# Kernel optimization log

Hardware: AMD Instinct MI355X
Metric: run time of the kernel (lower is better)

## Reference

```python
import jax, jax.numpy as jnp
import numpy as np

N_NODES = 100000
N_EDGES = 1_600_000
IN_CH = 64
HID = 128
OUT_CH = 2


def _glorot(key, shape):
    fan_in = shape[0]
    return jax.random.normal(key, shape, dtype=jnp.float32) / jnp.sqrt(jnp.float32(fan_in))


def setup_inputs() -> dict:
    key = jax.random.key(0)
    ks = jax.random.split(key, 10)
    x = jax.random.normal(ks[0], (N_NODES, IN_CH), dtype=jnp.float32)
    edge_index = jax.random.randint(ks[1], (2, N_EDGES), 0, N_NODES, dtype=jnp.int64)
    # SAGEConv layer 0: lin_l (neighbor, with bias) + lin_r (root)
    W_n0 = _glorot(ks[2], (IN_CH, HID))
    W_s0 = _glorot(ks[3], (IN_CH, HID))
    b0 = jnp.zeros((HID,), dtype=jnp.float32)
    # SAGEConv layer 1
    W_n1 = _glorot(ks[4], (HID, HID))
    W_s1 = _glorot(ks[5], (HID, HID))
    b1 = jnp.zeros((HID,), dtype=jnp.float32)
    # final fc
    fc_w = _glorot(ks[6], (HID, OUT_CH))
    fc_b = jnp.zeros((OUT_CH,), dtype=jnp.float32)
    return {"x": x, "edge_index": edge_index, "W_n0": W_n0, "W_s0": W_s0, "b0": b0,
            "W_n1": W_n1, "W_s1": W_s1, "b1": b1, "fc_w": fc_w, "fc_b": fc_b}


def _sage_conv(h, src, dst, W_n, W_s, b, num_nodes):
    # mean aggregation of source features onto destination nodes
    agg = jax.ops.segment_sum(h[src], dst, num_segments=num_nodes)  # [N, d]
    cnt = jax.ops.segment_sum(jnp.ones_like(dst, dtype=h.dtype), dst, num_segments=num_nodes)
    mean = agg / jnp.maximum(cnt, 1.0)[:, None]
    return mean @ W_n + h @ W_s + b


def reference(x, edge_index, W_n0, W_s0, b0, W_n1, W_s1, b1, fc_w, fc_b):
    src, dst = edge_index[0], edge_index[1]
    n = x.shape[0]
    h = jax.nn.relu(_sage_conv(x, src, dst, W_n0, W_s0, b0, n))  # dropout is identity in eval mode
    h = jax.nn.relu(_sage_conv(h, src, dst, W_n1, W_s1, b1, n))
    return h @ fc_w + fc_b
```

## Files before the change

### kernel.cpp

```cpp
#include <hip/hip_runtime.h>

#define N_NODES 100000
#define IN_CH 64
#define HID 128
#define BSH 8
#define NBUCK ((N_NODES + 255) >> 8)
#define NCB 512

typedef short short8 __attribute__((ext_vector_type(8)));
typedef float floatx4 __attribute__((ext_vector_type(4)));
typedef float floatx2 __attribute__((ext_vector_type(2)));

__device__ __forceinline__ unsigned short f2bf(float f) {
    unsigned u = __builtin_bit_cast(unsigned, f);
    u += 0x7fffu + ((u >> 16) & 1u);
    return (unsigned short)(u >> 16);
}

template <int K>
__device__ __forceinline__ void pack_dev(const float* __restrict__ Wn,
                                         const float* __restrict__ Ws,
                                         unsigned short* __restrict__ Bpack, int idx) {
    int s = idx >> 9;
    int rem = idx & 511;
    int t = rem >> 6;
    int lane = rem & 63;
    int quad = lane >> 4;
    int n = t * 16 + (lane & 15);
    unsigned short v[8];
#pragma unroll
    for (int j = 0; j < 8; ++j) {
        int k = s * 32 + quad * 8 + j;
        float w = (k < K) ? Wn[(size_t)k * HID + n] : Ws[(size_t)(k - K) * HID + n];
        v[j] = f2bf(w);
    }
    *(short8*)(Bpack + (size_t)idx * 8) = *(short8*)v;
}

__global__ __launch_bounds__(256) void histprep_kernel(const int* __restrict__ dst,
                                                       int* __restrict__ table, int E, int chunk,
                                                       const float* __restrict__ x,
                                                       unsigned short* __restrict__ x_bf,
                                                       unsigned char* __restrict__ x_f8,
                                                       const float* __restrict__ Wn0,
                                                       const float* __restrict__ Ws0,
                                                       unsigned short* __restrict__ Bpack0,
                                                       const float* __restrict__ Wn1,
                                                       const float* __restrict__ Ws1,
                                                       unsigned short* __restrict__ Bpack1,
                                                       int* __restrict__ scan_done, int n4) {
    int b = blockIdx.x;
    if (b < NCB) {
        if (b == 0 && threadIdx.x == 0) *scan_done = 0;
        __shared__ int h[NBUCK];
        for (int i = threadIdx.x; i < NBUCK; i += 256) h[i] = 0;
        __syncthreads();
        int e0 = b * chunk;
        int e1 = min(E, e0 + chunk);
        for (int e = e0 + threadIdx.x; e < e1; e += 256) atomicAdd(&h[dst[e] >> BSH], 1);
        __syncthreads();
        for (int i = threadIdx.x; i < NBUCK; i += 256) table[i * NCB + b] = h[i];
    } else if (b < NCB + 8) {
        pack_dev<IN_CH>(Wn0, Ws0, Bpack0, (b - NCB) * 256 + threadIdx.x);
    } else if (b < NCB + 24) {
        pack_dev<HID>(Wn1, Ws1, Bpack1, (b - NCB - 8) * 256 + threadIdx.x);
    } else {
        int i = (b - NCB - 24) * 256 + threadIdx.x;
        if (i < n4) {
            float4 v = ((const float4*)x)[i];
            ushort4 o;
            o.x = f2bf(v.x); o.y = f2bf(v.y); o.z = f2bf(v.z); o.w = f2bf(v.w);
            ((ushort4*)x_bf)[i] = o;
            int p8 = __builtin_amdgcn_cvt_pk_fp8_f32(v.x, v.y, 0, false);
            p8 = __builtin_amdgcn_cvt_pk_fp8_f32(v.z, v.w, p8, true);
            ((unsigned*)x_f8)[i] = (unsigned)p8;
        }
    }
}

__global__ __launch_bounds__(256) void scan12_kernel(int* __restrict__ table,
                                                     int* __restrict__ tot,
                                                     int* __restrict__ bstart,
                                                     int* __restrict__ ptr,
                                                     int* __restrict__ scan_done, int E) {
    __shared__ int s[256];
    __shared__ int lastflag;
    int b = blockIdx.x, t = threadIdx.x;
    int c0 = table[b * NCB + 2 * t];
    int c1 = table[b * NCB + 2 * t + 1];
    int s2 = c0 + c1;
    s[t] = s2;
    __syncthreads();
#pragma unroll
    for (int off = 1; off < 256; off <<= 1) {
        int v = (t >= off) ? s[t - off] : 0;
        __syncthreads();
        s[t] += v;
        __syncthreads();
    }
    int excl2 = s[t] - s2;
    table[b * NCB + 2 * t] = excl2;
    table[b * NCB + 2 * t + 1] = excl2 + c0;
    if (t == 255) {
        __hip_atomic_store(&tot[b], s[255], __ATOMIC_RELAXED, __HIP_MEMORY_SCOPE_AGENT);
        int prev = __hip_atomic_fetch_add(scan_done, 1, __ATOMIC_ACQ_REL, __HIP_MEMORY_SCOPE_AGENT);
        lastflag = (prev == NBUCK - 1);
    }
    __syncthreads();
    if (!lastflag) return;
    int v0 = (2 * t < NBUCK)
                 ? __hip_atomic_load(&tot[2 * t], __ATOMIC_RELAXED, __HIP_MEMORY_SCOPE_AGENT) : 0;
    int v1 = (2 * t + 1 < NBUCK)
                 ? __hip_atomic_load(&tot[2 * t + 1], __ATOMIC_RELAXED, __HIP_MEMORY_SCOPE_AGENT) : 0;
    int p2 = v0 + v1;
    __syncthreads();
    s[t] = p2;
    __syncthreads();
#pragma unroll
    for (int off = 1; off < 256; off <<= 1) {
        int u = (t >= off) ? s[t - off] : 0;
        __syncthreads();
        s[t] += u;
        __syncthreads();
    }
    int e2 = s[t] - p2;
    if (2 * t < NBUCK) bstart[2 * t] = e2;
    if (2 * t + 1 < NBUCK) bstart[2 * t + 1] = e2 + v0;
    if (t == 0) {
        bstart[NBUCK] = E;
        ptr[N_NODES] = E;
    }
}

__global__ __launch_bounds__(256) void bin_kernel(const int* __restrict__ src,
                                                  const int* __restrict__ dst,
                                                  const int* __restrict__ table,
                                                  const int* __restrict__ bstart,
                                                  unsigned* __restrict__ binned, int E, int chunk) {
    __shared__ int cur[NBUCK];
    int blk = blockIdx.x;
    for (int i = threadIdx.x; i < NBUCK; i += 256) cur[i] = bstart[i] + table[i * NCB + blk];
    __syncthreads();
    int e0 = blk * chunk;
    int e1 = min(E, e0 + chunk);
    for (int e = e0 + threadIdx.x; e < e1; e += 256) {
        int d = dst[e];
        int b = d >> BSH;
        int pos = atomicAdd(&cur[b], 1);
        if ((unsigned)pos < (unsigned)E)
            binned[pos] = (unsigned)src[e] | ((unsigned)(d & 255) << 17);
    }
}

__global__ __launch_bounds__(256) void place_kernel(const unsigned* __restrict__ binned,
                                                    const int* __restrict__ bstart,
                                                    int* __restrict__ ptr,
                                                    int* __restrict__ sorted, int N, int E) {
    __shared__ int deg[256];
    __shared__ int cur[256];
    __shared__ int ssum[256];
    int b = blockIdx.x, t = threadIdx.x;
    int start = bstart[b], end = bstart[b + 1];
    start = max(0, min(start, E));
    end = max(start, min(end, E));
    deg[t] = 0;
    __syncthreads();
    for (int i = start + t; i < end; i += 256) atomicAdd(&deg[(binned[i] >> 17) & 255], 1);
    __syncthreads();
    int a = deg[t];
    ssum[t] = a;
    __syncthreads();
#pragma unroll
    for (int off = 1; off < 256; off <<= 1) {
        int u = (t >= off) ? ssum[t - off] : 0;
        __syncthreads();
        ssum[t] += u;
        __syncthreads();
    }
    int excl = ssum[t] - a;
    cur[t] = excl;
    int n0 = b * 256 + t;
    if (n0 < N) ptr[n0] = start + excl;
    __syncthreads();
    for (int i = start + t; i < end; i += 256) {
        unsigned p = binned[i];
        int dl = (p >> 17) & 255;
        int pos = start + atomicAdd(&cur[dl], 1);
        if ((unsigned)pos < (unsigned)E) sorted[pos] = (int)(p & 0x1FFFF);
    }
}

template <int C>
__global__ __launch_bounds__(256) void gather_mean_w16p(const int* __restrict__ ptr,
                                                        const int* __restrict__ srcs,
                                                        const unsigned char* __restrict__ feat,
                                                        unsigned short* __restrict__ mean, int N,
                                                        int E) {
    constexpr int R = C / 16;
    constexpr int LOGR = (C == 64) ? 2 : 3;
    constexpr int NPW = 64 / R;
    const int lane = threadIdx.x & 63;
    const int g = lane >> LOGR;
    const int l = lane & (R - 1);
    const int w = (blockIdx.x * 4 + (threadIdx.x >> 6)) * NPW + g;
    if (w >= N) return;
    int s0 = ptr[w], s1 = ptr[w + 1];
    s0 = max(0, min(s0, E));
    s1 = max(s0, min(s1, E));
    const int deg = min(s1 - s0, 4096);

    floatx2 accq[4][8];
#pragma unroll
    for (int q = 0; q < 4; ++q)
#pragma unroll
        for (int u = 0; u < 8; ++u) { accq[q][u][0] = 0.0f; accq[q][u][1] = 0.0f; }

    const int nfull = deg & ~3;
    int j = 0;
    if (nfull > 0) {
        int cidn[4];
        uint4 v[4];
        {
            int cid0[4];
#pragma unroll
            for (int q = 0; q < 4; ++q)
                cid0[q] = (int)min((unsigned)srcs[s0 + q], (unsigned)(N_NODES - 1));
#pragma unroll
            for (int q = 0; q < 4; ++q)
                v[q] = *(const uint4*)(feat + (size_t)cid0[q] * C + l * 16);
            int base1 = (4 < nfull) ? s0 + 4 : s0;
#pragma unroll
            for (int q = 0; q < 4; ++q)
                cidn[q] = (int)min((unsigned)srcs[base1 + q], (unsigned)(N_NODES - 1));
        }
        for (; j < nfull; j += 4) {
            uint4 vn[4];
#pragma unroll
            for (int q = 0; q < 4; ++q)
                vn[q] = *(const uint4*)(feat + (size_t)cidn[q] * C + l * 16);
            int base2 = (j + 8 < nfull) ? s0 + j + 8 : s0;
            int cid2[4];
#pragma unroll
            for (int q = 0; q < 4; ++q)
                cid2[q] = (int)min((unsigned)srcs[base2 + q], (unsigned)(N_NODES - 1));
#pragma unroll
            for (int q = 0; q < 4; ++q) {
                const uint dw[4] = {v[q].x, v[q].y, v[q].z, v[q].w};
#pragma unroll
                for (int d = 0; d < 4; ++d) {
                    accq[q][2 * d + 0] += __builtin_amdgcn_cvt_pk_f32_fp8(dw[d], false);
                    accq[q][2 * d + 1] += __builtin_amdgcn_cvt_pk_f32_fp8(dw[d], true);
                }
            }
#pragma unroll
            for (int q = 0; q < 4; ++q) { v[q] = vn[q]; cidn[q] = cid2[q]; }
        }
    }
    if (j < deg) {
        int cid[4];
#pragma unroll
        for (int q = 0; q < 4; ++q) {
            int jj = min(j + q, deg - 1);
            cid[q] = (int)min((unsigned)srcs[s0 + jj], (unsigned)(N_NODES - 1));
        }
        uint4 v[4];
#pragma unroll
        for (int q = 0; q < 4; ++q)
            v[q] = *(const uint4*)(feat + (size_t)cid[q] * C + l * 16);
#pragma unroll
        for (int q = 0; q < 4; ++q) {
            uint dw[4] = {v[q].x, v[q].y, v[q].z, v[q].w};
#pragma unroll
            for (int d = 0; d < 4; ++d) dw[d] = (j + q < deg) ? dw[d] : 0u;
#pragma unroll
            for (int d = 0; d < 4; ++d) {
                accq[q][2 * d + 0] += __builtin_amdgcn_cvt_pk_f32_fp8(dw[d], false);
                accq[q][2 * d + 1] += __builtin_amdgcn_cvt_pk_f32_fp8(dw[d], true);
            }
        }
    }
#pragma unroll
    for (int u = 0; u < 8; ++u) {
        accq[0][u] += accq[1][u];
        accq[2][u] += accq[3][u];
        accq[0][u] += accq[2][u];
    }
    const float inv = (deg > 0) ? 1.0f / (float)deg : 0.0f;
    unsigned short o[16];
#pragma unroll
    for (int u = 0; u < 8; ++u) {
        o[2 * u + 0] = f2bf(accq[0][u][0] * inv);
        o[2 * u + 1] = f2bf(accq[0][u][1] * inv);
    }
    unsigned short* mp = mean + (size_t)w * C + l * 16;
    *(uint4*)(mp + 0) = ((const uint4*)o)[0];
    *(uint4*)(mp + 8) = ((const uint4*)o)[1];
}

template <int KT, bool FUSE_FC>
__global__ __launch_bounds__(256) void sage_gemm_mfma(const unsigned short* __restrict__ meanb,
                                                      const unsigned short* __restrict__ hb,
                                                      const unsigned short* __restrict__ Bpack,
                                                      const float* __restrict__ bias,
                                                      const float* __restrict__ fcw,
                                                      const float* __restrict__ fcb,
                                                      unsigned short* __restrict__ outb,
                                                      unsigned char* __restrict__ out8,
                                                      float* __restrict__ outf, int N) {
    constexpr int KH = KT / 2;
    constexpr int LDA = KT + 8;
    __shared__ unsigned short As[64 * LDA];
    const int t = threadIdx.x;
    const int row0 = blockIdx.x * 64;

    constexpr int SEGS = KT / 8;
    for (int c = t; c < 64 * SEGS; c += 256) {
        int r = c / SEGS, seg = c % SEGS;
        int rsrc = row0 + r;
        if (rsrc >= N) rsrc = N - 1;
        const unsigned short* srcp = (seg < SEGS / 2)
                                         ? meanb + (size_t)rsrc * KH + seg * 8
                                         : hb + (size_t)rsrc * KH + (seg - SEGS / 2) * 8;
        *(uint4*)&As[r * LDA + seg * 8] = *(const uint4*)srcp;
    }
    __syncthreads();

    const int lane = t & 63;
    const int wave = t >> 6;
    const int quad = lane >> 4;
    const int lo = lane & 15;

    floatx4 acc[8];
#pragma unroll
    for (int i = 0; i < 8; ++i)
#pragma unroll
        for (int r = 0; r < 4; ++r) acc[i][r] = 0.0f;

    const unsigned short* abase = &As[(wave * 16 + lo) * LDA + quad * 8];
#pragma unroll
    for (int s = 0; s < KT / 32; ++s) {
        short8 a = *(const short8*)(abase + s * 32);
        const short8* bp = (const short8*)Bpack + (size_t)(s * 8) * 64 + lane;
#pragma unroll
        for (int tt = 0; tt < 8; ++tt) {
            short8 b = bp[tt * 64];
            acc[tt] = __builtin_amdgcn_mfma_f32_16x16x32_bf16(a, b, acc[tt], 0, 0, 0);
        }
    }

    if (!FUSE_FC) {
        __syncthreads();
#pragma unroll
        for (int tt = 0; tt < 8; ++tt) {
            int col = tt * 16 + lo;
            float bv = bias[col];
#pragma unroll
            for (int r = 0; r < 4; ++r) {
                int rl = wave * 16 + quad * 4 + r;
                As[rl * LDA + col] = f2bf(fmaxf(acc[tt][r] + bv, 0.0f));
            }
        }
        __syncthreads();
        for (int i = t; i < 64 * (HID / 8); i += 256) {
            int r = i >> 4, ch = i & 15;
            int row = row0 + r;
            if (row < N)
                *(uint4*)(outb + (size_t)row * HID + ch * 8) = *(const uint4*)&As[r * LDA + ch * 8];
        }
        __syncthreads();
        unsigned char* As8 = (unsigned char*)As;
#pragma unroll
        for (int tt = 0; tt < 8; ++tt) {
            int col = tt * 16 + lo;
            float bv = bias[col];
#pragma unroll
            for (int r = 0; r < 4; ++r) {
                int rl = wave * 16 + quad * 4 + r;
                float v = fmaxf(acc[tt][r] + bv, 0.0f);
                int p8 = __builtin_amdgcn_cvt_pk_fp8_f32(v, v, 0, false);
                As8[rl * (LDA * 2) + col] = (unsigned char)(p8 & 0xff);
            }
        }
        __syncthreads();
        for (int i = t; i < 64 * (HID / 16); i += 256) {
            int r = i >> 3, ch = i & 7;
            int row = row0 + r;
            if (row < N)
                *(uint4*)(out8 + (size_t)row * HID + ch * 16) =
                    *(const uint4*)&As8[r * (LDA * 2) + ch * 16];
        }
    } else {
        float o0[4] = {}, o1[4] = {};
#pragma unroll
        for (int tt = 0; tt < 8; ++tt) {
            int col = tt * 16 + lo;
            float bv = bias[col];
            float w0 = fcw[col * 2 + 0];
            float w1 = fcw[col * 2 + 1];
#pragma unroll
            for (int r = 0; r < 4; ++r) {
                float v = fmaxf(acc[tt][r] + bv, 0.0f);
                o0[r] += v * w0;
                o1[r] += v * w1;
            }
        }
#pragma unroll
        for (int r = 0; r < 4; ++r) {
#pragma unroll
            for (int m = 8; m >= 1; m >>= 1) {
                o0[r] += __shfl_xor(o0[r], m, 16);
                o1[r] += __shfl_xor(o1[r], m, 16);
            }
        }
        if (lo == 0) {
#pragma unroll
            for (int r = 0; r < 4; ++r) {
                int row = row0 + wave * 16 + quad * 4 + r;
                if (row < N) {
                    outf[(size_t)row * 2 + 0] = o0[r] + fcb[0];
                    outf[(size_t)row * 2 + 1] = o1[r] + fcb[1];
                }
            }
        }
    }
}

extern "C" void kernel_launch(void* const* d_in, const int* in_sizes, int n_in,
                              void* d_out, int out_size, void* d_ws, size_t ws_size,
                              hipStream_t stream) {
    const float* x   = (const float*)d_in[0];
    const int*   ei  = (const int*)d_in[1];
    const float* Wn0 = (const float*)d_in[2];
    const float* Ws0 = (const float*)d_in[3];
    const float* b0  = (const float*)d_in[4];
    const float* Wn1 = (const float*)d_in[5];
    const float* Ws1 = (const float*)d_in[6];
    const float* b1  = (const float*)d_in[7];
    const float* fcw = (const float*)d_in[8];
    const float* fcb = (const float*)d_in[9];
    float* out = (float*)d_out;

    const int E = in_sizes[1] / 2;
    const int* src = ei;
    const int* dst = ei + E;
    const int N = N_NODES;
    const int chunk = (E + NCB - 1) / NCB;

    char* ws = (char*)d_ws;
    size_t off = 0;
    int* table  = (int*)(ws + off); off += (size_t)NBUCK * NCB * 4;
    int* tot    = (int*)(ws + off); off += 4096;
    int* bstart = (int*)(ws + off); off += 4096;
    int* scan_done = (int*)(ws + off); off += 256;
    int* ptr    = (int*)(ws + off); off += (size_t)(N + 1) * 4 + 60; off &= ~(size_t)63;
    unsigned* binned = (unsigned*)(ws + off); off += (size_t)E * 4;
    int* sorted = (int*)(ws + off); off += (size_t)E * 4;
    off = (off + 255) & ~(size_t)255;
    unsigned short* x_bf   = (unsigned short*)(ws + off); off += (size_t)N * IN_CH * 2;
    unsigned short* mean0  = (unsigned short*)(ws + off); off += (size_t)N * IN_CH * 2;
    unsigned short* h1_bf  = (unsigned short*)(ws + off); off += (size_t)N * HID * 2;
    unsigned short* mean1  = (unsigned short*)(ws + off); off += (size_t)N * HID * 2;
    unsigned char*  h1_f8  = (unsigned char*)(ws + off);  off += (size_t)N * HID;
    unsigned char*  x_f8   = (unsigned char*)(ws + off);  off += (size_t)N * IN_CH;
    off = (off + 255) & ~(size_t)255;
    unsigned short* Bpack0 = (unsigned short*)(ws + off); off += (size_t)(2 * IN_CH / 32) * 8 * 64 * 8 * 2;
    unsigned short* Bpack1 = (unsigned short*)(ws + off); off += (size_t)(2 * HID / 32) * 8 * 64 * 8 * 2;

    {
        int n4 = N * IN_CH / 4;
        int nblk = NCB + 24 + (n4 + 255) / 256;
        histprep_kernel<<<nblk, 256, 0, stream>>>(dst, table, E, chunk, x, x_bf, x_f8,
                                                  Wn0, Ws0, Bpack0, Wn1, Ws1, Bpack1,
                                                  scan_done, n4);
    }
    scan12_kernel<<<NBUCK, 256, 0, stream>>>(table, tot, bstart, ptr, scan_done, E);
    bin_kernel<<<NCB, 256, 0, stream>>>(src, dst, table, bstart, binned, E, chunk);
    place_kernel<<<NBUCK, 256, 0, stream>>>(binned, bstart, ptr, sorted, N, E);

    gather_mean_w16p<IN_CH><<<(N + 63) / 64, 256, 0, stream>>>(ptr, sorted, x_f8, mean0, N, E);
    sage_gemm_mfma<2 * IN_CH, false><<<(N + 63) / 64, 256, 0, stream>>>(
        mean0, x_bf, Bpack0, b0, nullptr, nullptr, h1_bf, h1_f8, nullptr, N);

    gather_mean_w16p<HID><<<(N + 31) / 32, 256, 0, stream>>>(ptr, sorted, h1_f8, mean1, N, E);
    sage_gemm_mfma<2 * HID, true><<<(N + 63) / 64, 256, 0, stream>>>(
        mean1, h1_bf, Bpack1, b1, fcw, fcb, nullptr, nullptr, out, N);
}
```

Measured before the change: 232.3 us.

## Replace two-level bucket sort CSR build with global-atomic count, alloc, scatter

```diff
diff --git a/kernel.cpp b/kernel.cpp
--- a/kernel.cpp
+++ b/kernel.cpp
@@ -3,9 +3,9 @@
 #define N_NODES 100000
 #define IN_CH 64
 #define HID 128
-#define BSH 8
-#define NBUCK ((N_NODES + 255) >> 8)
-#define NCB 512
+#define NCC 512
+#define ZB ((N_NODES + 1023) >> 10)
+#define NAB ((N_NODES + 255) >> 8)
 
 typedef short short8 __attribute__((ext_vector_type(8)));
 typedef float floatx4 __attribute__((ext_vector_type(4)));
@@ -37,35 +37,28 @@
     *(short8*)(Bpack + (size_t)idx * 8) = *(short8*)v;
 }
 
-__global__ __launch_bounds__(256) void histprep_kernel(const int* __restrict__ dst,
-                                                       int* __restrict__ table, int E, int chunk,
-                                                       const float* __restrict__ x,
-                                                       unsigned short* __restrict__ x_bf,
-                                                       unsigned char* __restrict__ x_f8,
-                                                       const float* __restrict__ Wn0,
-                                                       const float* __restrict__ Ws0,
-                                                       unsigned short* __restrict__ Bpack0,
-                                                       const float* __restrict__ Wn1,
-                                                       const float* __restrict__ Ws1,
-                                                       unsigned short* __restrict__ Bpack1,
-                                                       int* __restrict__ scan_done, int n4) {
+__global__ __launch_bounds__(256) void prep_kernel(const float* __restrict__ x,
+                                                   unsigned short* __restrict__ x_bf,
+                                                   unsigned char* __restrict__ x_f8,
+                                                   const float* __restrict__ Wn0,
+                                                   const float* __restrict__ Ws0,
+                                                   unsigned short* __restrict__ Bpack0,
+                                                   const float* __restrict__ Wn1,
+                                                   const float* __restrict__ Ws1,
+                                                   unsigned short* __restrict__ Bpack1,
+                                                   int* __restrict__ degcnt,
+                                                   int* __restrict__ gcur, int n4) {
     int b = blockIdx.x;
-    if (b < NCB) {
-        if (b == 0 && threadIdx.x == 0) *scan_done = 0;
-        __shared__ int h[NBUCK];
-        for (int i = threadIdx.x; i < NBUCK; i += 256) h[i] = 0;
-        __syncthreads();
-        int e0 = b * chunk;
-        int e1 = min(E, e0 + chunk);
-        for (int e = e0 + threadIdx.x; e < e1; e += 256) atomicAdd(&h[dst[e] >> BSH], 1);
-        __syncthreads();
-        for (int i = threadIdx.x; i < NBUCK; i += 256) table[i * NCB + b] = h[i];
-    } else if (b < NCB + 8) {
-        pack_dev<IN_CH>(Wn0, Ws0, Bpack0, (b - NCB) * 256 + threadIdx.x);
-    } else if (b < NCB + 24) {
-        pack_dev<HID>(Wn1, Ws1, Bpack1, (b - NCB - 8) * 256 + threadIdx.x);
+    if (b < ZB) {
+        if (b == 0 && threadIdx.x == 0) *gcur = 0;
+        int i = (b * 256 + threadIdx.x) * 4;
+        *(int4*)(degcnt + i) = make_int4(0, 0, 0, 0);
+    } else if (b < ZB + 8) {
+        pack_dev<IN_CH>(Wn0, Ws0, Bpack0, (b - ZB) * 256 + threadIdx.x);
+    } else if (b < ZB + 24) {
+        pack_dev<HID>(Wn1, Ws1, Bpack1, (b - ZB - 8) * 256 + threadIdx.x);
     } else {
-        int i = (b - NCB - 24) * 256 + threadIdx.x;
+        int i = (b - ZB - 24) * 256 + threadIdx.x;
         if (i < n4) {
             float4 v = ((const float4*)x)[i];
             ushort4 o;
@@ -78,120 +71,57 @@
     }
 }
 
-__global__ __launch_bounds__(256) void scan12_kernel(int* __restrict__ table,
-                                                     int* __restrict__ tot,
-                                                     int* __restrict__ bstart,
-                                                     int* __restrict__ ptr,
-                                                     int* __restrict__ scan_done, int E) {
-    __shared__ int s[256];
-    __shared__ int lastflag;
-    int b = blockIdx.x, t = threadIdx.x;
-    int c0 = table[b * NCB + 2 * t];
-    int c1 = table[b * NCB + 2 * t + 1];
-    int s2 = c0 + c1;
-    s[t] = s2;
+__global__ __launch_bounds__(256) void count_kernel(const int* __restrict__ dst,
+                                                    int* __restrict__ degcnt, int E, int chunk) {
+    int e0 = blockIdx.x * chunk;
+    int e1 = min(E, e0 + chunk);
+    for (int e = e0 + threadIdx.x; e < e1; e += 256) atomicAdd(&degcnt[dst[e]], 1);
+}
+
+__global__ __launch_bounds__(256) void alloc_kernel(const int* __restrict__ degcnt,
+                                                    int* __restrict__ gcur,
+                                                    int* __restrict__ ptr,
+                                                    int* __restrict__ cur, int N) {
+    __shared__ int ssum[256];
+    __shared__ int sbase;
+    int t = threadIdx.x;
+    int n = blockIdx.x * 256 + t;
+    int d = (n < N) ? degcnt[n] : 0;
+    d = max(0, min(d, 65535));
+    ssum[t] = d;
     __syncthreads();
 #pragma unroll
     for (int off = 1; off < 256; off <<= 1) {
-        int v = (t >= off) ? s[t - off] : 0;
-        __syncthreads();
-        s[t] += v;
-        __syncthreads();
-    }
-    int excl2 = s[t] - s2;
-    table[b * NCB + 2 * t] = excl2;
-    table[b * NCB + 2 * t + 1] = excl2 + c0;
-    if (t == 255) {
-        __hip_atomic_store(&tot[b], s[255], __ATOMIC_RELAXED, __HIP_MEMORY_SCOPE_AGENT);
-        int prev = __hip_atomic_fetch_add(scan_done, 1, __ATOMIC_ACQ_REL, __HIP_MEMORY_SCOPE_AGENT);
-        lastflag = (prev == NBUCK - 1);
-    }
+        int u = (t >= off) ? ssum[t - off] : 0;
+        __syncthreads();
+        ssum[t] += u;
+        __syncthreads();
+    }
+    int excl = ssum[t] - d;
+    if (t == 255) sbase = atomicAdd(gcur, ssum[255]);
     __syncthreads();
-    if (!lastflag) return;
-    int v0 = (2 * t < NBUCK)
-                 ? __hip_atomic_load(&tot[2 * t], __ATOMIC_RELAXED, __HIP_MEMORY_SCOPE_AGENT) : 0;
-    int v1 = (2 * t + 1 < NBUCK)
-                 ? __hip_atomic_load(&tot[2 * t + 1], __ATOMIC_RELAXED, __HIP_MEMORY_SCOPE_AGENT) : 0;
-    int p2 = v0 + v1;
-    __syncthreads();
-    s[t] = p2;
-    __syncthreads();
-#pragma unroll
-    for (int off = 1; off < 256; off <<= 1) {
-        int u = (t >= off) ? s[t - off] : 0;
-        __syncthreads();
-        s[t] += u;
-        __syncthreads();
-    }
-    int e2 = s[t] - p2;
-    if (2 * t < NBUCK) bstart[2 * t] = e2;
-    if (2 * t + 1 < NBUCK) bstart[2 * t + 1] = e2 + v0;
-    if (t == 0) {
-        bstart[NBUCK] = E;
-        ptr[N_NODES] = E;
-    }
-}
-
-__global__ __launch_bounds__(256) void bin_kernel(const int* __restrict__ src,
-                                                  const int* __restrict__ dst,
-                                                  const int* __restrict__ table,
-                                                  const int* __restrict__ bstart,
-                                                  unsigned* __restrict__ binned, int E, int chunk) {
-    __shared__ int cur[NBUCK];
-    int blk = blockIdx.x;
-    for (int i = threadIdx.x; i < NBUCK; i += 256) cur[i] = bstart[i] + table[i * NCB + blk];
-    __syncthreads();
-    int e0 = blk * chunk;
+    int p = sbase + excl;
+    if (n < N) {
+        ptr[n] = p;
+        cur[n] = p;
+    }
+}
+
+__global__ __launch_bounds__(256) void scatter_kernel(const int* __restrict__ src,
+                                                      const int* __restrict__ dst,
+                                                      int* __restrict__ cur,
+                                                      int* __restrict__ sorted, int E, int chunk) {
+    int e0 = blockIdx.x * chunk;
     int e1 = min(E, e0 + chunk);
     for (int e = e0 + threadIdx.x; e < e1; e += 256) {
-        int d = dst[e];
-        int b = d >> BSH;
-        int pos = atomicAdd(&cur[b], 1);
-        if ((unsigned)pos < (unsigned)E)
-            binned[pos] = (unsigned)src[e] | ((unsigned)(d & 255) << 17);
-    }
-}
-
-__global__ __launch_bounds__(256) void place_kernel(const unsigned* __restrict__ binned,
-                                                    const int* __restrict__ bstart,
-                                                    int* __restrict__ ptr,
-                                                    int* __restrict__ sorted, int N, int E) {
-    __shared__ int deg[256];
-    __shared__ int cur[256];
-    __shared__ int ssum[256];
-    int b = blockIdx.x, t = threadIdx.x;
-    int start = bstart[b], end = bstart[b + 1];
-    start = max(0, min(start, E));
-    end = max(start, min(end, E));
-    deg[t] = 0;
-    __syncthreads();
-    for (int i = start + t; i < end; i += 256) atomicAdd(&deg[(binned[i] >> 17) & 255], 1);
-    __syncthreads();
-    int a = deg[t];
-    ssum[t] = a;
-    __syncthreads();
-#pragma unroll
-    for (int off = 1; off < 256; off <<= 1) {
-        int u = (t >= off) ? ssum[t - off] : 0;
-        __syncthreads();
-        ssum[t] += u;
-        __syncthreads();
-    }
-    int excl = ssum[t] - a;
-    cur[t] = excl;
-    int n0 = b * 256 + t;
-    if (n0 < N) ptr[n0] = start + excl;
-    __syncthreads();
-    for (int i = start + t; i < end; i += 256) {
-        unsigned p = binned[i];
-        int dl = (p >> 17) & 255;
-        int pos = start + atomicAdd(&cur[dl], 1);
-        if ((unsigned)pos < (unsigned)E) sorted[pos] = (int)(p & 0x1FFFF);
+        int pos = atomicAdd(&cur[dst[e]], 1);
+        if ((unsigned)pos < (unsigned)E) sorted[pos] = src[e];
     }
 }
 
 template <int C>
 __global__ __launch_bounds__(256) void gather_mean_w16p(const int* __restrict__ ptr,
+                                                        const int* __restrict__ degcnt,
                                                         const int* __restrict__ srcs,
                                                         const unsigned char* __restrict__ feat,
                                                         unsigned short* __restrict__ mean, int N,
@@ -204,10 +134,10 @@
     const int l = lane & (R - 1);
     const int w = (blockIdx.x * 4 + (threadIdx.x >> 6)) * NPW + g;
     if (w >= N) return;
-    int s0 = ptr[w], s1 = ptr[w + 1];
+    int s0 = ptr[w];
     s0 = max(0, min(s0, E));
-    s1 = max(s0, min(s1, E));
-    const int deg = min(s1 - s0, 4096);
+    int deg = degcnt[w];
+    deg = max(0, min(min(deg, 4096), E - s0));
 
     floatx2 accq[4][8];
 #pragma unroll
@@ -444,16 +374,14 @@
     const int* src = ei;
     const int* dst = ei + E;
     const int N = N_NODES;
-    const int chunk = (E + NCB - 1) / NCB;
+    const int chunk = (E + NCC - 1) / NCC;
 
     char* ws = (char*)d_ws;
     size_t off = 0;
-    int* table  = (int*)(ws + off); off += (size_t)NBUCK * NCB * 4;
-    int* tot    = (int*)(ws + off); off += 4096;
-    int* bstart = (int*)(ws + off); off += 4096;
-    int* scan_done = (int*)(ws + off); off += 256;
-    int* ptr    = (int*)(ws + off); off += (size_t)(N + 1) * 4 + 60; off &= ~(size_t)63;
-    unsigned* binned = (unsigned*)(ws + off); off += (size_t)E * 4;
+    int* degcnt = (int*)(ws + off); off += (size_t)ZB * 1024 * 4;
+    int* gcur   = (int*)(ws + off); off += 256;
+    int* ptr    = (int*)(ws + off); off += (size_t)N * 4 + 252; off &= ~(size_t)255;
+    int* cur    = (int*)(ws + off); off += (size_t)N * 4 + 252; off &= ~(size_t)255;
     int* sorted = (int*)(ws + off); off += (size_t)E * 4;
     off = (off + 255) & ~(size_t)255;
     unsigned short* x_bf   = (unsigned short*)(ws + off); off += (size_t)N * IN_CH * 2;
@@ -468,20 +396,21 @@
 
     {
         int n4 = N * IN_CH / 4;
-        int nblk = NCB + 24 + (n4 + 255) / 256;
-        histprep_kernel<<<nblk, 256, 0, stream>>>(dst, table, E, chunk, x, x_bf, x_f8,
-                                                  Wn0, Ws0, Bpack0, Wn1, Ws1, Bpack1,
-                                                  scan_done, n4);
-    }
-    scan12_kernel<<<NBUCK, 256, 0, stream>>>(table, tot, bstart, ptr, scan_done, E);
-    bin_kernel<<<NCB, 256, 0, stream>>>(src, dst, table, bstart, binned, E, chunk);
-    place_kernel<<<NBUCK, 256, 0, stream>>>(binned, bstart, ptr, sorted, N, E);
-
-    gather_mean_w16p<IN_CH><<<(N + 63) / 64, 256, 0, stream>>>(ptr, sorted, x_f8, mean0, N, E);
+        int nblk = ZB + 24 + (n4 + 255) / 256;
+        prep_kernel<<<nblk, 256, 0, stream>>>(x, x_bf, x_f8, Wn0, Ws0, Bpack0,
+                                              Wn1, Ws1, Bpack1, degcnt, gcur, n4);
+    }
+    count_kernel<<<NCC, 256, 0, stream>>>(dst, degcnt, E, chunk);
+    alloc_kernel<<<NAB, 256, 0, stream>>>(degcnt, gcur, ptr, cur, N);
+    scatter_kernel<<<NCC, 256, 0, stream>>>(src, dst, cur, sorted, E, chunk);
+
+    gather_mean_w16p<IN_CH><<<(N + 63) / 64, 256, 0, stream>>>(ptr, degcnt, sorted, x_f8, mean0,
+                                                               N, E);
     sage_gemm_mfma<2 * IN_CH, false><<<(N + 63) / 64, 256, 0, stream>>>(
         mean0, x_bf, Bpack0, b0, nullptr, nullptr, h1_bf, h1_f8, nullptr, N);
 
-    gather_mean_w16p<HID><<<(N + 31) / 32, 256, 0, stream>>>(ptr, sorted, h1_f8, mean1, N, E);
+    gather_mean_w16p<HID><<<(N + 31) / 32, 256, 0, stream>>>(ptr, degcnt, sorted, h1_f8, mean1,
+                                                             N, E);
     sage_gemm_mfma<2 * HID, true><<<(N + 63) / 64, 256, 0, stream>>>(
         mean1, h1_bf, Bpack1, b1, fcw, fcb, nullptr, nullptr, out, N);
 }
```

New measurement: 381.7 us. 64.3% more time.
